# Performance work log

Hardware: AMD Instinct MI355X
Metric: run time of the kernel (lower is better)

## Reference

```python
import jax, jax.numpy as jnp
import numpy as np

NUM_USERS = 100000
NUM_ITEMS = 50000
N_NODES = NUM_USERS + NUM_ITEMS
D = 64
N_LAYERS = 3
E = 2000000
B = 1024
ALPHA_PREF = 1.0


def setup_inputs() -> dict:
    key = jax.random.key(0)
    k1, k2, k3, k4 = jax.random.split(key, 4)
    embed = jax.random.normal(k1, (N_NODES, D), dtype=jnp.float32) * 0.1
    edge_index = jax.random.randint(k2, (2, E), 0, N_NODES, dtype=jnp.int32)
    users = jax.random.randint(k3, (B,), 0, NUM_USERS, dtype=jnp.int32)
    items = jax.random.randint(k4, (B,), 0, NUM_ITEMS, dtype=jnp.int32)
    return {"embed": embed, "edge_index": edge_index, "users": users, "items": items}


def _lightgcn_propagate(x, row, col, norm):
    # message: norm * x[row] (x_j = source), aggregated (add) at col (target)
    msg = norm[:, None] * x[row]                      # [E, D]
    return jnp.zeros_like(x).at[col].add(msg)         # [N, D]


def reference(embed, edge_index, users, items):
    row, col = edge_index[0], edge_index[1]
    n = embed.shape[0]
    # degree normalization (depends only on edge_index; same every layer)
    deg = jnp.zeros((n,), jnp.float32).at[row].add(1.0)
    deg_inv = jnp.clip(deg, 1.0, None) ** -0.5
    norm = deg_inv[row] * deg_inv[col]                # [E]

    x = embed
    for _ in range(N_LAYERS):
        x = _lightgcn_propagate(x, row, col, norm)

    u_emb = x[users]                                  # [B, D]
    i_emb = x[items + NUM_USERS]                      # [B, D]

    # mask = (row == users[:,None]) flattened selection of col; edge e is
    # selected once per batch element b with users[b] == row[e] -> multiplicity
    cnt = jnp.zeros((n,), jnp.float32).at[users].add(1.0)
    mult = cnt[row]                                   # [E] selection multiplicity

    # PreferenceShapley surrogate: softmax over selected neighbor embeddings
    # of alpha_pref * <neigh_emb, mean(u_emb)>, flattened over the batch.
    context = u_emb.mean(0)                           # [D]
    neigh = x[col]                                    # [E, D]
    logits = ALPHA_PREF * (neigh @ context)           # [E]
    masked = jnp.where(mult > 0, logits, -jnp.inf)
    mx = jnp.max(masked)
    ew = mult * jnp.exp(logits - mx)                  # [E] weighted exp (0 where unselected)
    z = jnp.clip(ew.sum(), 1e-12, None)
    neigh_aggr = (ew[:, None] * neigh).sum(0) / z     # [D]

    score = (u_emb * i_emb).sum(-1) + u_emb @ neigh_aggr  # [B]
    return jax.nn.sigmoid(score)
```

## Files before the change

### kernel.cpp

```cpp
#include <hip/hip_runtime.h>
#include <float.h>
#include <math.h>

#define NUM_USERS 100000
#define NUM_ITEMS 50000
#define NNODES    150000
#define DIM       64
#define NEDGE     2000000
#define BATCH     1024
#define SEL_CAP   (1 << 18)
#define LOGIT_BLOCKS 512

#define SLICES   1024
#define EPS      1956
#define NBUK     293

__device__ __forceinline__ float wave_sum64(float v) {
    #pragma unroll
    for (int off = 32; off > 0; off >>= 1) v += __shfl_xor(v, off, 64);
    return v;
}

__device__ __forceinline__ float bf2f(unsigned short s) {
    return __uint_as_float(((unsigned int)s) << 16);
}
__device__ __forceinline__ unsigned short f2bf(float f) {
    unsigned int u = __float_as_uint(f);
    return (unsigned short)((u + 0x7fffu + ((u >> 16) & 1u)) >> 16);
}


__global__ __launch_bounds__(512) void bhist_kernel(
        const int* __restrict__ row, const int* __restrict__ col,
        const int* __restrict__ ucnt,
        unsigned short* __restrict__ cntR, unsigned short* __restrict__ cntC,
        int* __restrict__ n_sel, int* __restrict__ sel_col, float* __restrict__ sel_w) {
    __shared__ unsigned int hr[NBUK], hc[NBUK];
    __shared__ int lcnt, lbase;
    __shared__ int2 buf[256];
    int blk = blockIdx.x, t = threadIdx.x;
    for (int i = t; i < NBUK; i += 512) { hr[i] = 0; hc[i] = 0; }
    if (t == 0) lcnt = 0;
    __syncthreads();
    int e0 = blk * EPS;
    int e1 = e0 + EPS; if (e1 > NEDGE) e1 = NEDGE;
    for (int base = e0 + t * 4; base < e1; base += 2048) {
        if (base + 4 <= e1) {
            int4 r4 = *(const int4*)(row + base);
            int4 c4 = *(const int4*)(col + base);
            atomicAdd(&hr[r4.x >> 9], 1u);
            atomicAdd(&hr[r4.y >> 9], 1u);
            atomicAdd(&hr[r4.z >> 9], 1u);
            atomicAdd(&hr[r4.w >> 9], 1u);
            atomicAdd(&hc[c4.x >> 9], 1u);
            atomicAdd(&hc[c4.y >> 9], 1u);
            atomicAdd(&hc[c4.z >> 9], 1u);
            atomicAdd(&hc[c4.w >> 9], 1u);
            int u0 = ucnt[r4.x], u1 = ucnt[r4.y], u2 = ucnt[r4.z], u3 = ucnt[r4.w];
            if (u0 > 0) { int i = atomicAdd(&lcnt, 1); if (i < 256) buf[i] = make_int2(c4.x, u0); }
            if (u1 > 0) { int i = atomicAdd(&lcnt, 1); if (i < 256) buf[i] = make_int2(c4.y, u1); }
            if (u2 > 0) { int i = atomicAdd(&lcnt, 1); if (i < 256) buf[i] = make_int2(c4.z, u2); }
            if (u3 > 0) { int i = atomicAdd(&lcnt, 1); if (i < 256) buf[i] = make_int2(c4.w, u3); }
        } else {
            for (int e = base; e < e1; ++e) {
                int r = row[e], c = col[e];
                atomicAdd(&hr[r >> 9], 1u);
                atomicAdd(&hc[c >> 9], 1u);
                int u = ucnt[r];
                if (u > 0) { int i = atomicAdd(&lcnt, 1); if (i < 256) buf[i] = make_int2(c, u); }
            }
        }
    }
    __syncthreads();
    for (int i = t; i < NBUK; i += 512) {
        cntR[(size_t)blk * NBUK + i] = (unsigned short)hr[i];
        cntC[(size_t)blk * NBUK + i] = (unsigned short)hc[i];
    }
    if (t == 0) {
        int c = lcnt; c = c < 256 ? c : 256;
        lbase = atomicAdd(n_sel, c);
    }
    __syncthreads();
    int c = lcnt; c = c < 256 ? c : 256;
    int b = lbase;
    for (int i = t; i < c; i += 512) {
        int o = b + i;
        if (o < SEL_CAP) { sel_col[o] = buf[i].x; sel_w[o] = (float)buf[i].y; }
    }
}


__global__ __launch_bounds__(512) void bprefix1_kernel(
        const unsigned short* __restrict__ cntR, const unsigned short* __restrict__ cntC,
        unsigned short* __restrict__ offR, unsigned short* __restrict__ offC,
        int* __restrict__ totRC) {
    int side = blockIdx.x / NBUK;
    int b = blockIdx.x - side * NBUK;
    const unsigned short* cnt = side ? cntC : cntR;
    unsigned short* off = side ? offC : offR;
    __shared__ int sm[512];
    int t = threadIdx.x;
    int v0 = (int)cnt[(size_t)(2 * t) * NBUK + b];
    int v1 = (int)cnt[(size_t)(2 * t + 1) * NBUK + b];
    int p = v0 + v1;
    sm[t] = p;
    __syncthreads();
    for (int o = 1; o < 512; o <<= 1) {
        int x = (t >= o) ? sm[t - o] : 0;
        __syncthreads();
        sm[t] += x;
        __syncthreads();
    }
    int excl = sm[t] - p;
    off[(size_t)(2 * t) * NBUK + b]     = (unsigned short)excl;
    off[(size_t)(2 * t + 1) * NBUK + b] = (unsigned short)(excl + v0);
    if (t == 511) totRC[side * NBUK + b] = sm[511];
}

__global__ __launch_bounds__(512) void bprefix2_kernel(
        const int* __restrict__ totRC, int* __restrict__ baseR, int* __restrict__ baseC) {
    const int* tot = totRC + blockIdx.x * NBUK;
    int* base = blockIdx.x ? baseC : baseR;
    __shared__ int sm[512];
    int t = threadIdx.x;
    int v = (t < NBUK) ? tot[t] : 0;
    sm[t] = v;
    __syncthreads();
    for (int o = 1; o < 512; o <<= 1) {
        int x = (t >= o) ? sm[t - o] : 0;
        __syncthreads();
        sm[t] += x;
        __syncthreads();
    }
    if (t < NBUK) base[t] = sm[t] - v;
    if (t == NBUK - 1) base[NBUK] = sm[t];
}


__global__ __launch_bounds__(512) void place_kernel(
        const int* __restrict__ row, const int* __restrict__ col,
        const unsigned short* __restrict__ cntR, const unsigned short* __restrict__ cntC,
        const unsigned short* __restrict__ offR, const unsigned short* __restrict__ offC,
        const int* __restrict__ baseR, const int* __restrict__ baseC,
        unsigned short* __restrict__ midR, unsigned int* __restrict__ midC) {
    __shared__ int lofC[NBUK], lofR[NBUK], posC[NBUK], posR[NBUK];
    __shared__ int cCl[NBUK], cRl[NBUK];
    __shared__ unsigned int hrP[NBUK], hcP[NBUK];
    __shared__ int scan_tmp[512];
    __shared__ unsigned int   stC[EPS];
    __shared__ unsigned short stR[EPS];
    __shared__ unsigned short bmapC[EPS], bmapR[EPS];
    int blk = blockIdx.x, t = threadIdx.x;
    if (t < NBUK) {
        cCl[t] = (int)cntC[(size_t)blk * NBUK + t];
        cRl[t] = (int)cntR[(size_t)blk * NBUK + t];
        posC[t] = baseC[t] + (int)offC[(size_t)blk * NBUK + t];
        posR[t] = baseR[t] + (int)offR[(size_t)blk * NBUK + t];
    }
    __syncthreads();
    scan_tmp[t] = (t < NBUK) ? cCl[t] : 0;
    __syncthreads();
    for (int o = 1; o < 512; o <<= 1) {
        int v = (t >= o) ? scan_tmp[t - o] : 0;
        __syncthreads();
        scan_tmp[t] += v;
        __syncthreads();
    }
    if (t < NBUK) lofC[t] = scan_tmp[t] - cCl[t];
    __syncthreads();
    scan_tmp[t] = (t < NBUK) ? cRl[t] : 0;
    __syncthreads();
    for (int o = 1; o < 512; o <<= 1) {
        int v = (t >= o) ? scan_tmp[t - o] : 0;
        __syncthreads();
        scan_tmp[t] += v;
        __syncthreads();
    }
    if (t < NBUK) lofR[t] = scan_tmp[t] - cRl[t];
    __syncthreads();
    if (t < NBUK) {
        int c = cCl[t], lo = lofC[t];
        for (int k = 0; k < c; ++k) bmapC[lo + k] = (unsigned short)t;
        c = cRl[t]; lo = lofR[t];
        for (int k = 0; k < c; ++k) bmapR[lo + k] = (unsigned short)t;
    }
    for (int i = t; i < NBUK; i += 512) { hrP[i] = 0; hcP[i] = 0; }
    __syncthreads();
    int e0 = blk * EPS;
    int e1 = e0 + EPS; if (e1 > NEDGE) e1 = NEDGE;
    for (int base = e0 + t * 4; base < e1; base += 2048) {
        if (base + 4 <= e1) {
            int4 r4 = *(const int4*)(row + base);
            int4 c4 = *(const int4*)(col + base);
            unsigned int kc0 = atomicAdd(&hcP[c4.x >> 9], 1u);
            unsigned int kc1 = atomicAdd(&hcP[c4.y >> 9], 1u);
            unsigned int kc2 = atomicAdd(&hcP[c4.z >> 9], 1u);
            unsigned int kc3 = atomicAdd(&hcP[c4.w >> 9], 1u);
            stC[lofC[c4.x >> 9] + (int)kc0] = ((unsigned int)(c4.x & 511) << 18) | (unsigned int)r4.x;
            stC[lofC[c4.y >> 9] + (int)kc1] = ((unsigned int)(c4.y & 511) << 18) | (unsigned int)r4.y;
            stC[lofC[c4.z >> 9] + (int)kc2] = ((unsigned int)(c4.z & 511) << 18) | (unsigned int)r4.z;
            stC[lofC[c4.w >> 9] + (int)kc3] = ((unsigned int)(c4.w & 511) << 18) | (unsigned int)r4.w;
            unsigned int kr0 = atomicAdd(&hrP[r4.x >> 9], 1u);
            unsigned int kr1 = atomicAdd(&hrP[r4.y >> 9], 1u);
            unsigned int kr2 = atomicAdd(&hrP[r4.z >> 9], 1u);
            unsigned int kr3 = atomicAdd(&hrP[r4.w >> 9], 1u);
            stR[lofR[r4.x >> 9] + (int)kr0] = (unsigned short)(r4.x & 511);
            stR[lofR[r4.y >> 9] + (int)kr1] = (unsigned short)(r4.y & 511);
            stR[lofR[r4.z >> 9] + (int)kr2] = (unsigned short)(r4.z & 511);
            stR[lofR[r4.w >> 9] + (int)kr3] = (unsigned short)(r4.w & 511);
        } else {
            for (int e = base; e < e1; ++e) {
                int r = row[e], c = col[e];
                unsigned int kc = atomicAdd(&hcP[c >> 9], 1u);
                stC[lofC[c >> 9] + (int)kc] = ((unsigned int)(c & 511) << 18) | (unsigned int)r;
                unsigned int kr = atomicAdd(&hrP[r >> 9], 1u);
                stR[lofR[r >> 9] + (int)kr] = (unsigned short)(r & 511);
            }
        }
    }
    __syncthreads();
    int total = e1 - e0;
    for (int j = t; j < total; j += 512) {
        int b = bmapC[j];
        midC[posC[b] + (j - lofC[b])] = stC[j];
        b = bmapR[j];
        midR[posR[b] + (j - lofR[b])] = stR[j];
    }
}


__global__ __launch_bounds__(1024) void bfinal_kernel(
        const unsigned int* __restrict__ midC, const int* __restrict__ baseC,
        const unsigned short* __restrict__ midR, const int* __restrict__ baseR,
        const float4* __restrict__ embed,
        int* __restrict__ rptr, int* __restrict__ src_sorted,
        float* __restrict__ dinv, float* __restrict__ dinv2,
        uint2* __restrict__ y0) {
    __shared__ int cnt[512], sm[512], cur[512];
    __shared__ float dinvL[512];
    int b = blockIdx.x, t = threadIdx.x;
    int s0 = baseC[b], s1 = baseC[b + 1];
    if (t < 512) cnt[t] = 0;
    __syncthreads();
    for (int i = s0 + t; i < s1; i += 1024) atomicAdd(&cnt[midC[i] >> 18], 1);
    __syncthreads();
    if (t < 512) sm[t] = cnt[t];
    __syncthreads();
    for (int off = 1; off < 512; off <<= 1) {
        int v = 0;
        if (t < 512 && t >= off) v = sm[t - off];
        __syncthreads();
        if (t < 512) sm[t] += v;
        __syncthreads();
    }
    if (t < 512) {
        int excl = s0 + sm[t] - cnt[t];
        int n = b * 512 + t;
        if (n < NNODES) rptr[n] = excl;
        cur[t] = excl;
    }
    if (b == NBUK - 1 && t == 0) rptr[NNODES] = s1;
    if (b == 0 && t < 16) y0[(size_t)NNODES * 16 + t] = make_uint2(0u, 0u);
    __syncthreads();
    for (int i = s0 + t; i < s1; i += 1024) {
        unsigned int v = midC[i];
        int dst = atomicAdd(&cur[v >> 18], 1);
        src_sorted[dst] = (int)(v & 0x3FFFFu);
    }
    __syncthreads();
    if (t < 512) cnt[t] = 0;
    __syncthreads();
    int r0 = baseR[b], r1 = baseR[b + 1];
    for (int i = r0 + t; i < r1; i += 1024) atomicAdd(&cnt[midR[i]], 1);
    __syncthreads();
    if (t < 512) {
        int n = b * 512 + t;
        if (n < NNODES) {
            float d = fmaxf((float)cnt[t], 1.0f);
            float di = rsqrtf(d);
            dinv[n] = di; dinv2[n] = 1.0f / d;
            dinvL[t] = di;
        }
    }
    __syncthreads();
    int nbase = b * 512;
    int nmax = NNODES - nbase; if (nmax > 512) nmax = 512;
    if (nmax < 0) nmax = 0;
    for (int i = t; i < nmax * 16; i += 1024) {
        int ln = i >> 4, slot = i & 15;
        float d = dinvL[ln];
        float4 v = embed[(size_t)(nbase + ln) * 16 + slot];
        unsigned int w0 = (unsigned int)f2bf(v.x * d) | ((unsigned int)f2bf(v.y * d) << 16);
        unsigned int w1 = (unsigned int)f2bf(v.z * d) | ((unsigned int)f2bf(v.w * d) << 16);
        y0[(size_t)(nbase + ln) * 16 + slot] = make_uint2(w0, w1);
    }
}


#define ACC8(V) do { \
    a0 += __uint_as_float((V).x << 16); a1 += __uint_as_float((V).x & 0xffff0000u); \
    a2 += __uint_as_float((V).y << 16); a3 += __uint_as_float((V).y & 0xffff0000u); \
    a4 += __uint_as_float((V).z << 16); a5 += __uint_as_float((V).z & 0xffff0000u); \
    a6 += __uint_as_float((V).w << 16); a7 += __uint_as_float((V).w & 0xffff0000u); \
} while (0)

__device__ __forceinline__ void prop_node(
        const uint4* __restrict__ x_in, uint4* __restrict__ x_out,
        const int* __restrict__ ptr, const int* __restrict__ src,
        const float* __restrict__ scale, int node, int sl) {
    int i = ptr[node], e = ptr[node + 1];
    float sc = scale[node];
    float a0 = 0.f, a1 = 0.f, a2 = 0.f, a3 = 0.f;
    float a4 = 0.f, a5 = 0.f, a6 = 0.f, a7 = 0.f;
    int p0, p1, p2, p3;
    if (i + 4 <= e) { p0 = src[i]; p1 = src[i + 1]; p2 = src[i + 2]; p3 = src[i + 3]; }
    while (i + 8 <= e) {
        uint4 w0 = x_in[p0 * 8 + sl];
        uint4 w1 = x_in[p1 * 8 + sl];
        uint4 w2 = x_in[p2 * 8 + sl];
        uint4 w3 = x_in[p3 * 8 + sl];
        p0 = src[i + 4]; p1 = src[i + 5]; p2 = src[i + 6]; p3 = src[i + 7];
        i += 4;
        ACC8(w0); ACC8(w1); ACC8(w2); ACC8(w3);
    }
    if (i + 4 <= e) {
        uint4 w0 = x_in[p0 * 8 + sl];
        uint4 w1 = x_in[p1 * 8 + sl];
        uint4 w2 = x_in[p2 * 8 + sl];
        uint4 w3 = x_in[p3 * 8 + sl];
        i += 4;
        ACC8(w0); ACC8(w1); ACC8(w2); ACC8(w3);
    }
    if (i < e) {
        int q0 = src[i];
        int q1 = (i + 1 < e) ? src[i + 1] : NNODES;
        int q2 = (i + 2 < e) ? src[i + 2] : NNODES;
        uint4 w0 = x_in[q0 * 8 + sl];
        uint4 w1 = x_in[q1 * 8 + sl];
        uint4 w2 = x_in[q2 * 8 + sl];
        ACC8(w0); ACC8(w1); ACC8(w2);
    }
    uint4 o;
    o.x = (unsigned int)f2bf(a0 * sc) | ((unsigned int)f2bf(a1 * sc) << 16);
    o.y = (unsigned int)f2bf(a2 * sc) | ((unsigned int)f2bf(a3 * sc) << 16);
    o.z = (unsigned int)f2bf(a4 * sc) | ((unsigned int)f2bf(a5 * sc) << 16);
    o.w = (unsigned int)f2bf(a6 * sc) | ((unsigned int)f2bf(a7 * sc) << 16);
    x_out[(size_t)node * 8 + sl] = o;
}

__global__ __launch_bounds__(256, 8) void prop_kernel(
        const uint4* __restrict__ x_in, uint4* __restrict__ x_out,
        const int* __restrict__ ptr, const int* __restrict__ src,
        const float* __restrict__ scale) {
    int gid  = blockIdx.x * blockDim.x + threadIdx.x;
    int node = gid >> 3;
    int sl   = gid & 7;
    if (node > NNODES) return;
    if (node == NNODES) {
        x_out[(size_t)node * 8 + sl] = make_uint4(0u, 0u, 0u, 0u);
        return;
    }
    prop_node(x_in, x_out, ptr, src, scale, node, sl);
}

__global__ __launch_bounds__(256, 8) void prop_list_kernel(
        const uint4* __restrict__ x_in, uint4* __restrict__ x_out,
        const int* __restrict__ ptr, const int* __restrict__ src,
        const float* __restrict__ scale,
        const int* __restrict__ users, const int* __restrict__ items,
        const int* __restrict__ sel_col, const int* __restrict__ n_sel_p) {
    int n = *n_sel_p; if (n > SEL_CAP) n = SEL_CAP;
    int total = (2 * BATCH + n) * 8;
    int nth = gridDim.x * blockDim.x;
    for (int gid = blockIdx.x * blockDim.x + threadIdx.x; gid < total; gid += nth) {
        int li = gid >> 3;
        int sl = gid & 7;
        int node;
        if (li < BATCH) {
            node = users[li];
        } else if (li < 2 * BATCH) {
            node = items[li - BATCH] + NUM_USERS;
        } else {
            node = sel_col[li - 2 * BATCH];
        }
        prop_node(x_in, x_out, ptr, src, scale, node, sl);
    }
}


__global__ void ucnt_kernel(const int* __restrict__ users, int* __restrict__ ucnt) {
    int b = blockIdx.x * blockDim.x + threadIdx.x;
    if (b < BATCH) atomicAdd(&ucnt[users[b]], 1);
}

__global__ __launch_bounds__(256) void ctx_part_kernel(
        const unsigned short* __restrict__ x, const int* __restrict__ users,
        float* __restrict__ ctx) {
    __shared__ float sm[256];
    int lane = threadIdx.x & 63, wl = threadIdx.x >> 6;
    int b0 = blockIdx.x * 16 + wl * 4;
    float acc = 0.0f;
    #pragma unroll
    for (int k = 0; k < 4; ++k)
        acc += bf2f(x[users[b0 + k] * DIM + lane]);
    sm[threadIdx.x] = acc;
    __syncthreads();
    if (wl == 0)
        atomicAdd(&ctx[lane], sm[lane] + sm[64 + lane] + sm[128 + lane] + sm[192 + lane]);
}

__global__ void softmax_kernel(const unsigned short* __restrict__ x,
                               const float* __restrict__ ctx,
                               const int* __restrict__ sel_col,
                               const float* __restrict__ sel_w,
                               const int* __restrict__ n_sel_p,
                               float* __restrict__ S, float* __restrict__ zp) {
    __shared__ float smS[4 * 64];
    __shared__ float smZ[4];
    int lane = threadIdx.x & 63, wl = threadIdx.x >> 6;
    int n = *n_sel_p; if (n > SEL_CAP) n = SEL_CAP;
    float c = ctx[lane] * (1.0f / BATCH);
    float accS = 0.0f, accZ = 0.0f;
    int stride = gridDim.x * 4;
    for (int idx = blockIdx.x * 4 + wl; idx < n; idx += stride) {
        int node = sel_col[idx];
        float xv = bf2f(x[node * DIM + lane]);
        float v = wave_sum64(xv * c);
        float w = sel_w[idx] * __expf(v);
        accS = fmaf(w, xv, accS);
        accZ += w;
    }
    smS[wl * 64 + lane] = accS;
    if (lane == 0) smZ[wl] = accZ;
    __syncthreads();
    if (wl == 0) {
        float s = smS[lane] + smS[64 + lane] + smS[128 + lane] + smS[192 + lane];
        atomicAdd(&S[lane], s);
    }
    if (threadIdx.x == 0) atomicAdd(zp, smZ[0] + smZ[1] + smZ[2] + smZ[3]);
}

__global__ void score_kernel(const unsigned short* __restrict__ x, const int* __restrict__ users,
                             const int* __restrict__ items, const float* __restrict__ S,
                             const float* __restrict__ zp, float* __restrict__ out) {
    int gid = blockIdx.x * blockDim.x + threadIdx.x;
    int b = gid >> 6, lane = gid & 63;
    if (b >= BATCH) return;
    float z = fmaxf(*zp, 1e-12f);
    float na = S[lane] / z;
    int u = users[b], it = items[b] + NUM_USERS;
    float v = bf2f(x[u * DIM + lane]) * (bf2f(x[it * DIM + lane]) + na);
    v = wave_sum64(v);
    if (lane == 0) out[b] = 1.0f / (1.0f + __expf(-v));
}


extern "C" void kernel_launch(void* const* d_in, const int* in_sizes, int n_in,
                              void* d_out, int out_size, void* d_ws, size_t ws_size,
                              hipStream_t stream) {
    const float* embed = (const float*)d_in[0];
    const int*   edge  = (const int*)d_in[1];
    const int*   row   = edge;
    const int*   col   = edge + NEDGE;
    const int*   users = (const int*)d_in[2];
    const int*   items = (const int*)d_in[3];
    float*       out   = (float*)d_out;
    char*        ws    = (char*)d_ws;

    size_t off = 0;
    auto A = [&](size_t bytes) { size_t o = off; off += (bytes + 255) & ~(size_t)255; return o; };
    size_t o_mid   = A((size_t)NEDGE * 4 + (size_t)NEDGE * 2);
    size_t o_xa    = A((size_t)(NNODES + 1) * DIM * 2);
    size_t o_xb    = A((size_t)(NNODES + 1) * DIM * 2);
    size_t o_src   = A((size_t)NEDGE * 4);
    size_t o_cntR  = A((size_t)SLICES * NBUK * 2);
    size_t o_cntC  = A((size_t)SLICES * NBUK * 2);
    size_t o_offR  = A((size_t)SLICES * NBUK * 2);
    size_t o_offC  = A((size_t)SLICES * NBUK * 2);
    size_t o_tot   = A((size_t)2 * NBUK * 4);
    size_t o_baseR = A((size_t)(NBUK + 1) * 4);
    size_t o_baseC = A((size_t)(NBUK + 1) * 4);
    size_t o_selc  = A((size_t)SEL_CAP * 4);
    size_t o_selw  = A((size_t)SEL_CAP * 4);
    size_t o_zero  = off;
    size_t o_ucnt  = A((size_t)NNODES * 4);
    size_t o_misc  = A(1024);
    size_t zero_bytes = off - o_zero;
    size_t o_dinv  = A((size_t)NNODES * 4);
    size_t o_dinv2 = A((size_t)NNODES * 4);
    size_t o_rptr  = A((size_t)(NNODES + 1) * 4);

    unsigned int*   midC = (unsigned int*)(ws + o_mid);
    unsigned short* midR = (unsigned short*)(ws + o_mid + (size_t)NEDGE * 4);
    unsigned short* xa   = (unsigned short*)(ws + o_xa);
    unsigned short* xb   = (unsigned short*)(ws + o_xb);
    int*   srcS  = (int*)(ws + o_src);
    unsigned short* cntR = (unsigned short*)(ws + o_cntR);
    unsigned short* cntC = (unsigned short*)(ws + o_cntC);
    unsigned short* offR = (unsigned short*)(ws + o_offR);
    unsigned short* offC = (unsigned short*)(ws + o_offC);
    int*   totRC = (int*)(ws + o_tot);
    int*   baseR = (int*)(ws + o_baseR);
    int*   baseC = (int*)(ws + o_baseC);
    int*   selc  = (int*)(ws + o_selc);
    float* selw  = (float*)(ws + o_selw);
    int*   ucnt  = (int*)(ws + o_ucnt);
    int*   nsel  = (int*)(ws + o_misc);
    float* zp    = (float*)(ws + o_misc + 8);
    float* S     = (float*)(ws + o_misc + 256);
    float* ctx   = (float*)(ws + o_misc + 512);
    float* dinv  = (float*)(ws + o_dinv);
    float* dinv2 = (float*)(ws + o_dinv2);
    int*   rptr  = (int*)(ws + o_rptr);

    hipMemsetAsync(ws + o_zero, 0, zero_bytes, stream);

    ucnt_kernel<<<(BATCH + 255) / 256, 256, 0, stream>>>(users, ucnt);

    bhist_kernel<<<SLICES, 512, 0, stream>>>(row, col, ucnt, cntR, cntC,
                                             nsel, selc, selw);
    bprefix1_kernel<<<2 * NBUK, 512, 0, stream>>>(cntR, cntC, offR, offC, totRC);
    bprefix2_kernel<<<2, 512, 0, stream>>>(totRC, baseR, baseC);
    place_kernel<<<SLICES, 512, 0, stream>>>(row, col, cntR, cntC,
                                             offR, offC, baseR, baseC, midR, midC);
    bfinal_kernel<<<NBUK, 1024, 0, stream>>>(midC, baseC, midR, baseR,
                                             (const float4*)embed, rptr, srcS,
                                             dinv, dinv2, (uint2*)xa);

    int prop_blocks = ((NNODES + 1) * 8 + 255) / 256;
    prop_kernel<<<prop_blocks, 256, 0, stream>>>((const uint4*)xa, (uint4*)xb, rptr, srcS, dinv2);
    prop_kernel<<<prop_blocks, 256, 0, stream>>>((const uint4*)xb, (uint4*)xa, rptr, srcS, dinv2);
    prop_list_kernel<<<1024, 256, 0, stream>>>((const uint4*)xa, (uint4*)xb,
                                               rptr, srcS, dinv,
                                               users, items, selc, nsel);

    ctx_part_kernel<<<64, 256, 0, stream>>>(xb, users, ctx);
    softmax_kernel<<<LOGIT_BLOCKS, 256, 0, stream>>>(xb, ctx, selc, selw, nsel, S, zp);

    score_kernel<<<(BATCH * 64 + 255) / 256, 256, 0, stream>>>(xb, users, items, S, zp, out);
}
```

Measured before the change: 262.7 us.

## Replace multi-pass bucket counting sort with atomic reservation into fixed-capacity buckets

Removes the separate prefix-scan kernels and the second placement pass. The histogram kernel now reserves per-block slots in each bucket with global atomics and scatters edges directly into fixed-capacity (BCAP) bucket regions. CSR end pointers are stored explicitly because bucket regions are no longer contiguous. This saves launches and a pass over the edge arrays. In exchange, the global scatter writes lose shared-memory staging, and edges are silently dropped if any bucket exceeds its capacity.

```diff
diff --git a/kernel.cpp b/kernel.cpp
--- a/kernel.cpp
+++ b/kernel.cpp
@@ -14,6 +14,7 @@
 #define SLICES   1024
 #define EPS      1956
 #define NBUK     293
+#define BCAP     8192
 
 __device__ __forceinline__ float wave_sum64(float v) {
     #pragma unroll
@@ -30,12 +31,14 @@
 }
 
 
-__global__ __launch_bounds__(512) void bhist_kernel(
+__global__ __launch_bounds__(512) void sort_kernel(
         const int* __restrict__ row, const int* __restrict__ col,
         const int* __restrict__ ucnt,
-        unsigned short* __restrict__ cntR, unsigned short* __restrict__ cntC,
+        int* __restrict__ gcurC, int* __restrict__ gcurR,
+        unsigned int* __restrict__ midC, unsigned short* __restrict__ midR,
         int* __restrict__ n_sel, int* __restrict__ sel_col, float* __restrict__ sel_w) {
     __shared__ unsigned int hr[NBUK], hc[NBUK];
+    __shared__ int posC[NBUK], posR[NBUK];
     __shared__ int lcnt, lbase;
     __shared__ int2 buf[256];
     int blk = blockIdx.x, t = threadIdx.x;
@@ -72,10 +75,47 @@
         }
     }
     __syncthreads();
-    for (int i = t; i < NBUK; i += 512) {
-        cntR[(size_t)blk * NBUK + i] = (unsigned short)hr[i];
-        cntC[(size_t)blk * NBUK + i] = (unsigned short)hc[i];
-    }
+    if (t < NBUK) {
+        posC[t] = atomicAdd(&gcurC[t], (int)hc[t]);
+        posR[t] = atomicAdd(&gcurR[t], (int)hr[t]);
+        hc[t] = 0; hr[t] = 0;
+    }
+    __syncthreads();
+    for (int base = e0 + t * 4; base < e1; base += 2048) {
+        if (base + 4 <= e1) {
+            int4 r4 = *(const int4*)(row + base);
+            int4 c4 = *(const int4*)(col + base);
+            int b0 = c4.x >> 9, b1 = c4.y >> 9, b2 = c4.z >> 9, b3 = c4.w >> 9;
+            int k0 = posC[b0] + (int)atomicAdd(&hc[b0], 1u);
+            int k1 = posC[b1] + (int)atomicAdd(&hc[b1], 1u);
+            int k2 = posC[b2] + (int)atomicAdd(&hc[b2], 1u);
+            int k3 = posC[b3] + (int)atomicAdd(&hc[b3], 1u);
+            if (k0 < BCAP) midC[(size_t)b0 * BCAP + k0] = ((unsigned int)(c4.x & 511) << 18) | (unsigned int)r4.x;
+            if (k1 < BCAP) midC[(size_t)b1 * BCAP + k1] = ((unsigned int)(c4.y & 511) << 18) | (unsigned int)r4.y;
+            if (k2 < BCAP) midC[(size_t)b2 * BCAP + k2] = ((unsigned int)(c4.z & 511) << 18) | (unsigned int)r4.z;
+            if (k3 < BCAP) midC[(size_t)b3 * BCAP + k3] = ((unsigned int)(c4.w & 511) << 18) | (unsigned int)r4.w;
+            b0 = r4.x >> 9; b1 = r4.y >> 9; b2 = r4.z >> 9; b3 = r4.w >> 9;
+            k0 = posR[b0] + (int)atomicAdd(&hr[b0], 1u);
+            k1 = posR[b1] + (int)atomicAdd(&hr[b1], 1u);
+            k2 = posR[b2] + (int)atomicAdd(&hr[b2], 1u);
+            k3 = posR[b3] + (int)atomicAdd(&hr[b3], 1u);
+            if (k0 < BCAP) midR[(size_t)b0 * BCAP + k0] = (unsigned short)(r4.x & 511);
+            if (k1 < BCAP) midR[(size_t)b1 * BCAP + k1] = (unsigned short)(r4.y & 511);
+            if (k2 < BCAP) midR[(size_t)b2 * BCAP + k2] = (unsigned short)(r4.z & 511);
+            if (k3 < BCAP) midR[(size_t)b3 * BCAP + k3] = (unsigned short)(r4.w & 511);
+        } else {
+            for (int e = base; e < e1; ++e) {
+                int r = row[e], c = col[e];
+                int bc = c >> 9;
+                int kc = posC[bc] + (int)atomicAdd(&hc[bc], 1u);
+                if (kc < BCAP) midC[(size_t)bc * BCAP + kc] = ((unsigned int)(c & 511) << 18) | (unsigned int)r;
+                int br = r >> 9;
+                int kr = posR[br] + (int)atomicAdd(&hr[br], 1u);
+                if (kr < BCAP) midR[(size_t)br * BCAP + kr] = (unsigned short)(r & 511);
+            }
+        }
+    }
+    __syncthreads();
     if (t == 0) {
         int c = lcnt; c = c < 256 ? c : 256;
         lbase = atomicAdd(n_sel, c);
@@ -90,156 +130,19 @@
 }
 
 
-__global__ __launch_bounds__(512) void bprefix1_kernel(
-        const unsigned short* __restrict__ cntR, const unsigned short* __restrict__ cntC,
-        unsigned short* __restrict__ offR, unsigned short* __restrict__ offC,
-        int* __restrict__ totRC) {
-    int side = blockIdx.x / NBUK;
-    int b = blockIdx.x - side * NBUK;
-    const unsigned short* cnt = side ? cntC : cntR;
-    unsigned short* off = side ? offC : offR;
-    __shared__ int sm[512];
-    int t = threadIdx.x;
-    int v0 = (int)cnt[(size_t)(2 * t) * NBUK + b];
-    int v1 = (int)cnt[(size_t)(2 * t + 1) * NBUK + b];
-    int p = v0 + v1;
-    sm[t] = p;
-    __syncthreads();
-    for (int o = 1; o < 512; o <<= 1) {
-        int x = (t >= o) ? sm[t - o] : 0;
-        __syncthreads();
-        sm[t] += x;
-        __syncthreads();
-    }
-    int excl = sm[t] - p;
-    off[(size_t)(2 * t) * NBUK + b]     = (unsigned short)excl;
-    off[(size_t)(2 * t + 1) * NBUK + b] = (unsigned short)(excl + v0);
-    if (t == 511) totRC[side * NBUK + b] = sm[511];
-}
-
-__global__ __launch_bounds__(512) void bprefix2_kernel(
-        const int* __restrict__ totRC, int* __restrict__ baseR, int* __restrict__ baseC) {
-    const int* tot = totRC + blockIdx.x * NBUK;
-    int* base = blockIdx.x ? baseC : baseR;
-    __shared__ int sm[512];
-    int t = threadIdx.x;
-    int v = (t < NBUK) ? tot[t] : 0;
-    sm[t] = v;
-    __syncthreads();
-    for (int o = 1; o < 512; o <<= 1) {
-        int x = (t >= o) ? sm[t - o] : 0;
-        __syncthreads();
-        sm[t] += x;
-        __syncthreads();
-    }
-    if (t < NBUK) base[t] = sm[t] - v;
-    if (t == NBUK - 1) base[NBUK] = sm[t];
-}
-
-
-__global__ __launch_bounds__(512) void place_kernel(
-        const int* __restrict__ row, const int* __restrict__ col,
-        const unsigned short* __restrict__ cntR, const unsigned short* __restrict__ cntC,
-        const unsigned short* __restrict__ offR, const unsigned short* __restrict__ offC,
-        const int* __restrict__ baseR, const int* __restrict__ baseC,
-        unsigned short* __restrict__ midR, unsigned int* __restrict__ midC) {
-    __shared__ int lofC[NBUK], lofR[NBUK], posC[NBUK], posR[NBUK];
-    __shared__ int cCl[NBUK], cRl[NBUK];
-    __shared__ unsigned int hrP[NBUK], hcP[NBUK];
-    __shared__ int scan_tmp[512];
-    __shared__ unsigned int   stC[EPS];
-    __shared__ unsigned short stR[EPS];
-    __shared__ unsigned short bmapC[EPS], bmapR[EPS];
-    int blk = blockIdx.x, t = threadIdx.x;
-    if (t < NBUK) {
-        cCl[t] = (int)cntC[(size_t)blk * NBUK + t];
-        cRl[t] = (int)cntR[(size_t)blk * NBUK + t];
-        posC[t] = baseC[t] + (int)offC[(size_t)blk * NBUK + t];
-        posR[t] = baseR[t] + (int)offR[(size_t)blk * NBUK + t];
-    }
-    __syncthreads();
-    scan_tmp[t] = (t < NBUK) ? cCl[t] : 0;
-    __syncthreads();
-    for (int o = 1; o < 512; o <<= 1) {
-        int v = (t >= o) ? scan_tmp[t - o] : 0;
-        __syncthreads();
-        scan_tmp[t] += v;
-        __syncthreads();
-    }
-    if (t < NBUK) lofC[t] = scan_tmp[t] - cCl[t];
-    __syncthreads();
-    scan_tmp[t] = (t < NBUK) ? cRl[t] : 0;
-    __syncthreads();
-    for (int o = 1; o < 512; o <<= 1) {
-        int v = (t >= o) ? scan_tmp[t - o] : 0;
-        __syncthreads();
-        scan_tmp[t] += v;
-        __syncthreads();
-    }
-    if (t < NBUK) lofR[t] = scan_tmp[t] - cRl[t];
-    __syncthreads();
-    if (t < NBUK) {
-        int c = cCl[t], lo = lofC[t];
-        for (int k = 0; k < c; ++k) bmapC[lo + k] = (unsigned short)t;
-        c = cRl[t]; lo = lofR[t];
-        for (int k = 0; k < c; ++k) bmapR[lo + k] = (unsigned short)t;
-    }
-    for (int i = t; i < NBUK; i += 512) { hrP[i] = 0; hcP[i] = 0; }
-    __syncthreads();
-    int e0 = blk * EPS;
-    int e1 = e0 + EPS; if (e1 > NEDGE) e1 = NEDGE;
-    for (int base = e0 + t * 4; base < e1; base += 2048) {
-        if (base + 4 <= e1) {
-            int4 r4 = *(const int4*)(row + base);
-            int4 c4 = *(const int4*)(col + base);
-            unsigned int kc0 = atomicAdd(&hcP[c4.x >> 9], 1u);
-            unsigned int kc1 = atomicAdd(&hcP[c4.y >> 9], 1u);
-            unsigned int kc2 = atomicAdd(&hcP[c4.z >> 9], 1u);
-            unsigned int kc3 = atomicAdd(&hcP[c4.w >> 9], 1u);
-            stC[lofC[c4.x >> 9] + (int)kc0] = ((unsigned int)(c4.x & 511) << 18) | (unsigned int)r4.x;
-            stC[lofC[c4.y >> 9] + (int)kc1] = ((unsigned int)(c4.y & 511) << 18) | (unsigned int)r4.y;
-            stC[lofC[c4.z >> 9] + (int)kc2] = ((unsigned int)(c4.z & 511) << 18) | (unsigned int)r4.z;
-            stC[lofC[c4.w >> 9] + (int)kc3] = ((unsigned int)(c4.w & 511) << 18) | (unsigned int)r4.w;
-            unsigned int kr0 = atomicAdd(&hrP[r4.x >> 9], 1u);
-            unsigned int kr1 = atomicAdd(&hrP[r4.y >> 9], 1u);
-            unsigned int kr2 = atomicAdd(&hrP[r4.z >> 9], 1u);
-            unsigned int kr3 = atomicAdd(&hrP[r4.w >> 9], 1u);
-            stR[lofR[r4.x >> 9] + (int)kr0] = (unsigned short)(r4.x & 511);
-            stR[lofR[r4.y >> 9] + (int)kr1] = (unsigned short)(r4.y & 511);
-            stR[lofR[r4.z >> 9] + (int)kr2] = (unsigned short)(r4.z & 511);
-            stR[lofR[r4.w >> 9] + (int)kr3] = (unsigned short)(r4.w & 511);
-        } else {
-            for (int e = base; e < e1; ++e) {
-                int r = row[e], c = col[e];
-                unsigned int kc = atomicAdd(&hcP[c >> 9], 1u);
-                stC[lofC[c >> 9] + (int)kc] = ((unsigned int)(c & 511) << 18) | (unsigned int)r;
-                unsigned int kr = atomicAdd(&hrP[r >> 9], 1u);
-                stR[lofR[r >> 9] + (int)kr] = (unsigned short)(r & 511);
-            }
-        }
-    }
-    __syncthreads();
-    int total = e1 - e0;
-    for (int j = t; j < total; j += 512) {
-        int b = bmapC[j];
-        midC[posC[b] + (j - lofC[b])] = stC[j];
-        b = bmapR[j];
-        midR[posR[b] + (j - lofR[b])] = stR[j];
-    }
-}
-
-
 __global__ __launch_bounds__(1024) void bfinal_kernel(
-        const unsigned int* __restrict__ midC, const int* __restrict__ baseC,
-        const unsigned short* __restrict__ midR, const int* __restrict__ baseR,
+        const unsigned int* __restrict__ midC, const int* __restrict__ gcurC,
+        const unsigned short* __restrict__ midR, const int* __restrict__ gcurR,
         const float4* __restrict__ embed,
-        int* __restrict__ rptr, int* __restrict__ src_sorted,
+        int* __restrict__ rptr, int* __restrict__ rend, int* __restrict__ src_sorted,
         float* __restrict__ dinv, float* __restrict__ dinv2,
         uint2* __restrict__ y0) {
     __shared__ int cnt[512], sm[512], cur[512];
     __shared__ float dinvL[512];
     int b = blockIdx.x, t = threadIdx.x;
-    int s0 = baseC[b], s1 = baseC[b + 1];
+    int s0 = b * BCAP;
+    int cc = gcurC[b]; if (cc > BCAP) cc = BCAP;
+    int s1 = s0 + cc;
     if (t < 512) cnt[t] = 0;
     __syncthreads();
     for (int i = s0 + t; i < s1; i += 1024) atomicAdd(&cnt[midC[i] >> 18], 1);
@@ -256,10 +159,9 @@
     if (t < 512) {
         int excl = s0 + sm[t] - cnt[t];
         int n = b * 512 + t;
-        if (n < NNODES) rptr[n] = excl;
+        if (n < NNODES) { rptr[n] = excl; rend[n] = s0 + sm[t]; }
         cur[t] = excl;
     }
-    if (b == NBUK - 1 && t == 0) rptr[NNODES] = s1;
     if (b == 0 && t < 16) y0[(size_t)NNODES * 16 + t] = make_uint2(0u, 0u);
     __syncthreads();
     for (int i = s0 + t; i < s1; i += 1024) {
@@ -270,7 +172,9 @@
     __syncthreads();
     if (t < 512) cnt[t] = 0;
     __syncthreads();
-    int r0 = baseR[b], r1 = baseR[b + 1];
+    int r0 = b * BCAP;
+    int rc = gcurR[b]; if (rc > BCAP) rc = BCAP;
+    int r1 = r0 + rc;
     for (int i = r0 + t; i < r1; i += 1024) atomicAdd(&cnt[midR[i]], 1);
     __syncthreads();
     if (t < 512) {
@@ -306,9 +210,10 @@
 
 __device__ __forceinline__ void prop_node(
         const uint4* __restrict__ x_in, uint4* __restrict__ x_out,
-        const int* __restrict__ ptr, const int* __restrict__ src,
+        const int* __restrict__ ptr, const int* __restrict__ rend,
+        const int* __restrict__ src,
         const float* __restrict__ scale, int node, int sl) {
-    int i = ptr[node], e = ptr[node + 1];
+    int i = ptr[node], e = rend[node];
     float sc = scale[node];
     float a0 = 0.f, a1 = 0.f, a2 = 0.f, a3 = 0.f;
     float a4 = 0.f, a5 = 0.f, a6 = 0.f, a7 = 0.f;
@@ -350,7 +255,8 @@
 
 __global__ __launch_bounds__(256, 8) void prop_kernel(
         const uint4* __restrict__ x_in, uint4* __restrict__ x_out,
-        const int* __restrict__ ptr, const int* __restrict__ src,
+        const int* __restrict__ ptr, const int* __restrict__ rend,
+        const int* __restrict__ src,
         const float* __restrict__ scale) {
     int gid  = blockIdx.x * blockDim.x + threadIdx.x;
     int node = gid >> 3;
@@ -360,12 +266,13 @@
         x_out[(size_t)node * 8 + sl] = make_uint4(0u, 0u, 0u, 0u);
         return;
     }
-    prop_node(x_in, x_out, ptr, src, scale, node, sl);
+    prop_node(x_in, x_out, ptr, rend, src, scale, node, sl);
 }
 
 __global__ __launch_bounds__(256, 8) void prop_list_kernel(
         const uint4* __restrict__ x_in, uint4* __restrict__ x_out,
-        const int* __restrict__ ptr, const int* __restrict__ src,
+        const int* __restrict__ ptr, const int* __restrict__ rend,
+        const int* __restrict__ src,
         const float* __restrict__ scale,
         const int* __restrict__ users, const int* __restrict__ items,
         const int* __restrict__ sel_col, const int* __restrict__ n_sel_p) {
@@ -383,7 +290,7 @@
         } else {
             node = sel_col[li - 2 * BATCH];
         }
-        prop_node(x_in, x_out, ptr, src, scale, node, sl);
+        prop_node(x_in, x_out, ptr, rend, src, scale, node, sl);
     }
 }
 
@@ -469,42 +376,34 @@
 
     size_t off = 0;
     auto A = [&](size_t bytes) { size_t o = off; off += (bytes + 255) & ~(size_t)255; return o; };
-    size_t o_mid   = A((size_t)NEDGE * 4 + (size_t)NEDGE * 2);
+    size_t o_midC  = A((size_t)NBUK * BCAP * 4);
+    size_t o_midR  = A((size_t)NBUK * BCAP * 2);
     size_t o_xa    = A((size_t)(NNODES + 1) * DIM * 2);
     size_t o_xb    = A((size_t)(NNODES + 1) * DIM * 2);
-    size_t o_src   = A((size_t)NEDGE * 4);
-    size_t o_cntR  = A((size_t)SLICES * NBUK * 2);
-    size_t o_cntC  = A((size_t)SLICES * NBUK * 2);
-    size_t o_offR  = A((size_t)SLICES * NBUK * 2);
-    size_t o_offC  = A((size_t)SLICES * NBUK * 2);
-    size_t o_tot   = A((size_t)2 * NBUK * 4);
-    size_t o_baseR = A((size_t)(NBUK + 1) * 4);
-    size_t o_baseC = A((size_t)(NBUK + 1) * 4);
+    size_t o_src   = A((size_t)NBUK * BCAP * 4);
     size_t o_selc  = A((size_t)SEL_CAP * 4);
     size_t o_selw  = A((size_t)SEL_CAP * 4);
     size_t o_zero  = off;
     size_t o_ucnt  = A((size_t)NNODES * 4);
+    size_t o_gcurC = A((size_t)NBUK * 4);
+    size_t o_gcurR = A((size_t)NBUK * 4);
     size_t o_misc  = A(1024);
     size_t zero_bytes = off - o_zero;
     size_t o_dinv  = A((size_t)NNODES * 4);
     size_t o_dinv2 = A((size_t)NNODES * 4);
-    size_t o_rptr  = A((size_t)(NNODES + 1) * 4);
-
-    unsigned int*   midC = (unsigned int*)(ws + o_mid);
-    unsigned short* midR = (unsigned short*)(ws + o_mid + (size_t)NEDGE * 4);
+    size_t o_rptr  = A((size_t)NNODES * 4);
+    size_t o_rend  = A((size_t)NNODES * 4);
+
+    unsigned int*   midC = (unsigned int*)(ws + o_midC);
+    unsigned short* midR = (unsigned short*)(ws + o_midR);
     unsigned short* xa   = (unsigned short*)(ws + o_xa);
     unsigned short* xb   = (unsigned short*)(ws + o_xb);
     int*   srcS  = (int*)(ws + o_src);
-    unsigned short* cntR = (unsigned short*)(ws + o_cntR);
-    unsigned short* cntC = (unsigned short*)(ws + o_cntC);
-    unsigned short* offR = (unsigned short*)(ws + o_offR);
-    unsigned short* offC = (unsigned short*)(ws + o_offC);
-    int*   totRC = (int*)(ws + o_tot);
-    int*   baseR = (int*)(ws + o_baseR);
-    int*   baseC = (int*)(ws + o_baseC);
     int*   selc  = (int*)(ws + o_selc);
     float* selw  = (float*)(ws + o_selw);
     int*   ucnt  = (int*)(ws + o_ucnt);
+    int*   gcurC = (int*)(ws + o_gcurC);
+    int*   gcurR = (int*)(ws + o_gcurR);
     int*   nsel  = (int*)(ws + o_misc);
     float* zp    = (float*)(ws + o_misc + 8);
     float* S     = (float*)(ws + o_misc + 256);
@@ -512,26 +411,23 @@
     float* dinv  = (float*)(ws + o_dinv);
     float* dinv2 = (float*)(ws + o_dinv2);
     int*   rptr  = (int*)(ws + o_rptr);
+    int*   rend  = (int*)(ws + o_rend);
 
     hipMemsetAsync(ws + o_zero, 0, zero_bytes, stream);
 
     ucnt_kernel<<<(BATCH + 255) / 256, 256, 0, stream>>>(users, ucnt);
 
-    bhist_kernel<<<SLICES, 512, 0, stream>>>(row, col, ucnt, cntR, cntC,
-                                             nsel, selc, selw);
-    bprefix1_kernel<<<2 * NBUK, 512, 0, stream>>>(cntR, cntC, offR, offC, totRC);
-    bprefix2_kernel<<<2, 512, 0, stream>>>(totRC, baseR, baseC);
-    place_kernel<<<SLICES, 512, 0, stream>>>(row, col, cntR, cntC,
-                                             offR, offC, baseR, baseC, midR, midC);
-    bfinal_kernel<<<NBUK, 1024, 0, stream>>>(midC, baseC, midR, baseR,
-                                             (const float4*)embed, rptr, srcS,
+    sort_kernel<<<SLICES, 512, 0, stream>>>(row, col, ucnt, gcurC, gcurR,
+                                            midC, midR, nsel, selc, selw);
+    bfinal_kernel<<<NBUK, 1024, 0, stream>>>(midC, gcurC, midR, gcurR,
+                                             (const float4*)embed, rptr, rend, srcS,
                                              dinv, dinv2, (uint2*)xa);
 
     int prop_blocks = ((NNODES + 1) * 8 + 255) / 256;
-    prop_kernel<<<prop_blocks, 256, 0, stream>>>((const uint4*)xa, (uint4*)xb, rptr, srcS, dinv2);
-    prop_kernel<<<prop_blocks, 256, 0, stream>>>((const uint4*)xb, (uint4*)xa, rptr, srcS, dinv2);
+    prop_kernel<<<prop_blocks, 256, 0, stream>>>((const uint4*)xa, (uint4*)xb, rptr, rend, srcS, dinv2);
+    prop_kernel<<<prop_blocks, 256, 0, stream>>>((const uint4*)xb, (uint4*)xa, rptr, rend, srcS, dinv2);
     prop_list_kernel<<<1024, 256, 0, stream>>>((const uint4*)xa, (uint4*)xb,
-                                               rptr, srcS, dinv,
+                                               rptr, rend, srcS, dinv,
                                                users, items, selc, nsel);
 
     ctx_part_kernel<<<64, 256, 0, stream>>>(xb, users, ctx);
```

After: 261.5 us. Within noise of the previous version (-0.4%).
